# Kernel optimization log

Hardware: AMD Instinct MI355X
Metric: run time of the kernel (lower is better)

The kernel has to match this reference:

```python
import jax, jax.numpy as jnp
import numpy as np

N_HEADS, D_MODEL, D_HEAD = 16, 1024, 64
EPSILON = -100000.0  # module uses -1e5, not -inf
INIT_STD = 0.02


def setup_inputs() -> dict:
    key = jax.random.key(0)
    ks = jax.random.split(key, 5)
    B, S = 4, 2048
    x = jax.random.normal(ks[0], (B, S, D_MODEL), dtype=jnp.float32)
    W_Q = INIT_STD * jax.random.normal(ks[1], (N_HEADS, D_MODEL, D_HEAD), dtype=jnp.float32)
    W_K = INIT_STD * jax.random.normal(ks[2], (N_HEADS, D_MODEL, D_HEAD), dtype=jnp.float32)
    W_V = INIT_STD * jax.random.normal(ks[3], (N_HEADS, D_MODEL, D_HEAD), dtype=jnp.float32)
    W_O = INIT_STD * jax.random.normal(ks[4], (N_HEADS, D_HEAD, D_MODEL), dtype=jnp.float32)
    b_Q = jnp.zeros((N_HEADS, D_HEAD), jnp.float32)
    b_K = jnp.zeros((N_HEADS, D_HEAD), jnp.float32)
    b_V = jnp.zeros((N_HEADS, D_HEAD), jnp.float32)
    b_O = jnp.zeros((D_MODEL,), jnp.float32)
    return {"normalized_resid_pre": x, "W_Q": W_Q, "b_Q": b_Q, "W_K": W_K,
            "b_K": b_K, "W_V": W_V, "b_V": b_V, "W_O": W_O, "b_O": b_O}


def reference(normalized_resid_pre, W_Q, b_Q, W_K, b_K, W_V, b_V, W_O, b_O):
    x = normalized_resid_pre  # [b, s, e]
    q = jnp.einsum('bse,neh->bsnh', x, W_Q) + b_Q
    k = jnp.einsum('bse,neh->bsnh', x, W_K) + b_K
    v = jnp.einsum('bse,neh->bsnh', x, W_V) + b_V
    scores = jnp.einsum('bqnh,bknh->bnqk', q, k) / jnp.sqrt(jnp.float32(D_HEAD))
    sq, sk = scores.shape[-2], scores.shape[-1]
    causal = jnp.triu(jnp.ones((sq, sk), bool), k=1)  # True above diagonal
    scores = jnp.where(causal, jnp.float32(EPSILON), scores)
    probs = jax.nn.softmax(scores, axis=-1)
    z = jnp.einsum('bnqk,bknh->bqnh', probs, v)
    # sum over heads of per-head output projection + bias
    attn_out = jnp.einsum('bqnh,nhe->bqe', z, W_O) + b_O
    return attn_out
```

## Files before the change

### kernel.cpp

```cpp
#include <hip/hip_runtime.h>


typedef __attribute__((ext_vector_type(8))) short short8;
typedef __attribute__((ext_vector_type(4))) float floatx4;

#define SCL 0.1803368801111244f

__device__ __forceinline__ unsigned short f2bf(float f) {
  unsigned int x = __float_as_uint(f);
  x += 0x7fffu + ((x >> 16) & 1u);
  return (unsigned short)(x >> 16);
}

__device__ __forceinline__ void gload_lds16(const unsigned short* g, unsigned short* lds) {
  __builtin_amdgcn_global_load_lds(
      (const __attribute__((address_space(1))) void*)g,
      (__attribute__((address_space(3))) void*)lds, 16, 0, 0);
}

__global__ __launch_bounds__(256) void prep_kernel(
    const float* __restrict__ X,  unsigned short* __restrict__ Xb,
    const float* __restrict__ Wq, const float* __restrict__ Wk,
    const float* __restrict__ Wv, unsigned short* __restrict__ Bt,
    const float* __restrict__ Wo, unsigned short* __restrict__ Wt)
{
  __shared__ unsigned short T[64 * 72];
  const int bid = blockIdx.x, t = threadIdx.x;
  if (bid < 8192) {
    int idx = ((bid << 8) + t) << 2;
    float4 f = *(const float4*)(X + idx);
    unsigned short u[4] = { f2bf(f.x), f2bf(f.y), f2bf(f.z), f2bf(f.w) };
    *(uint2*)(Xb + idx) = *(uint2*)u;
  } else if (bid < 8960) {
    int b2 = bid - 8192;
    int e0 = (b2 & 15) << 6, nn = (b2 >> 4) & 15, proj = b2 >> 8;
    const float* W = (proj == 0) ? Wq : (proj == 1) ? Wk : Wv;
    const float* src = W + ((size_t)nn << 16) + ((size_t)e0 << 6);
#pragma unroll
    for (int rnd = 0; rnd < 4; ++rnd) {
      int off = (rnd << 10) + (t << 2);
      float4 f = *(const float4*)(src + off);
      int r = off >> 6, h = off & 63;
      T[r * 72 + h]     = f2bf(f.x);
      T[r * 72 + h + 1] = f2bf(f.y);
      T[r * 72 + h + 2] = f2bf(f.z);
      T[r * 72 + h + 3] = f2bf(f.w);
    }
    __syncthreads();
    const int h = t >> 2, ck = t & 3;
    size_t orow = ((size_t)((proj << 10) + (nn << 6) + h) << 10) + e0 + (ck << 4);
#pragma unroll
    for (int g = 0; g < 2; ++g) {
      unsigned short v[8];
#pragma unroll
      for (int j = 0; j < 8; ++j) v[j] = T[((ck << 4) + (g << 3) + j) * 72 + h];
      *(int4*)(Bt + orow + (g << 3)) = *(int4*)v;
    }
  } else {
    int b2 = bid - 8960;
    int e0 = (b2 & 15) << 6, k0 = (b2 >> 4) << 6;
#pragma unroll
    for (int rnd = 0; rnd < 4; ++rnd) {
      int r = (rnd << 4) + (t >> 4);
      int c = (t & 15) << 2;
      float4 f = *(const float4*)(Wo + ((size_t)(k0 + r) << 10) + e0 + c);
      T[r * 72 + c]     = f2bf(f.x);
      T[r * 72 + c + 1] = f2bf(f.y);
      T[r * 72 + c + 2] = f2bf(f.z);
      T[r * 72 + c + 3] = f2bf(f.w);
    }
    __syncthreads();
    const int i = t >> 2, ck = t & 3;
    size_t orow = ((size_t)(e0 + i) << 10) + k0 + (ck << 4);
#pragma unroll
    for (int g = 0; g < 2; ++g) {
      unsigned short v[8];
#pragma unroll
      for (int j = 0; j < 8; ++j) v[j] = T[((ck << 4) + (g << 3) + j) * 72 + i];
      *(int4*)(Wt + orow + (g << 3)) = *(int4*)v;
    }
  }
}

template <int MODE>
__global__ __launch_bounds__(256) void gemm128_kernel(
    const unsigned short* __restrict__ A,
    const unsigned short* __restrict__ Bt,
    const float* __restrict__ b0, const float* __restrict__ b1,
    const float* __restrict__ b2,
    unsigned short* __restrict__ Oq, unsigned short* __restrict__ Ok,
    unsigned short* __restrict__ Ov, float* __restrict__ Of)
{
  const int K = 1024;
  __shared__ __align__(16) unsigned short As[8192];
  __shared__ __align__(16) unsigned short Bs[8192];
  const int tid = threadIdx.x;
  const int l   = tid & 63, w = tid >> 6;
  const int l15 = l & 15,  lg = l >> 4;
  const int mo  = (w >> 1) << 6, no = (w & 1) << 6;
  const int m0  = blockIdx.y << 7, n0 = blockIdx.x << 7;
  const int srow = l >> 3;
  const int gblk = ((l & 7) ^ srow) << 3;
  const int rsw  = l15 & 7;

  floatx4 acc[4][4];
#pragma unroll
  for (int i = 0; i < 4; ++i)
#pragma unroll
    for (int j = 0; j < 4; ++j) acc[i][j] = (floatx4){0.f, 0.f, 0.f, 0.f};

  for (int k0 = 0; k0 < K; k0 += 64) {
    __syncthreads();
#pragma unroll
    for (int s = 0; s < 4; ++s) {
      const int br = (s << 5) + (w << 3);
      gload_lds16(A  + (size_t)(m0 + br + srow) * K + k0 + gblk, &As[br << 6]);
      gload_lds16(Bt + (size_t)(n0 + br + srow) * K + k0 + gblk, &Bs[br << 6]);
    }
    __syncthreads();
#pragma unroll
    for (int kh = 0; kh < 2; ++kh) {
      const int bo = (((kh << 2) + lg) ^ rsw) << 3;
      short8 af[4], bf[4];
#pragma unroll
      for (int mc = 0; mc < 4; ++mc)
        af[mc] = *(const short8*)&As[((mo + (mc << 4) + l15) << 6) + bo];
#pragma unroll
      for (int nc = 0; nc < 4; ++nc)
        bf[nc] = *(const short8*)&Bs[((no + (nc << 4) + l15) << 6) + bo];
#pragma unroll
      for (int mc = 0; mc < 4; ++mc)
#pragma unroll
        for (int nc = 0; nc < 4; ++nc)
          acc[mc][nc] = __builtin_amdgcn_mfma_f32_16x16x32_bf16(af[mc], bf[nc], acc[mc][nc], 0, 0, 0);
    }
  }

#pragma unroll
  for (int nc = 0; nc < 4; ++nc) {
    int c = n0 + no + (nc << 4) + l15;
    if (MODE == 1) {
      float bv = b0[c];
#pragma unroll
      for (int mc = 0; mc < 4; ++mc)
#pragma unroll
        for (int r = 0; r < 4; ++r) {
          int m = m0 + mo + (mc << 4) + (lg << 2) + r;
          Of[((size_t)m << 10) + c] = acc[mc][nc][r] + bv;
        }
    } else {
      int proj = c >> 10, cc = c & 1023;
      int hn = cc >> 6, h = cc & 63;
      const float* bp = (proj == 0) ? b0 : (proj == 1) ? b1 : b2;
      float bv = bp[cc];
      float sc = (proj == 0) ? SCL : 1.0f;
      if (proj < 2) {
        unsigned short* O = (proj == 0) ? Oq : Ok;
#pragma unroll
        for (int mc = 0; mc < 4; ++mc)
#pragma unroll
          for (int r = 0; r < 4; ++r) {
            int m = m0 + mo + (mc << 4) + (lg << 2) + r;
            int bb = m >> 11, ss = m & 2047;
            O[((((size_t)(bb << 4) + hn) << 11) + ss) * 64 + h] = f2bf((acc[mc][nc][r] + bv) * sc);
          }
      } else {
#pragma unroll
        for (int mc = 0; mc < 4; ++mc) {
          int m = m0 + mo + (mc << 4) + (lg << 2);
          int bb = m >> 11, ss = m & 2047;
          unsigned short p0 = f2bf(acc[mc][nc][0] + bv);
          unsigned short p1 = f2bf(acc[mc][nc][1] + bv);
          unsigned short p2 = f2bf(acc[mc][nc][2] + bv);
          unsigned short p3 = f2bf(acc[mc][nc][3] + bv);
          uint2 pk;
          pk.x = (unsigned int)p0 | ((unsigned int)p1 << 16);
          pk.y = (unsigned int)p2 | ((unsigned int)p3 << 16);
          *(uint2*)&Ov[((((size_t)(bb << 4) + hn) << 6) + h) * 2048 + ss] = pk;
        }
      }
    }
  }
}

__global__ __launch_bounds__(256, 4) void flash8_kernel(
    const unsigned short* __restrict__ Q,
    const unsigned short* __restrict__ K,
    const unsigned short* __restrict__ Vt,
    unsigned short* __restrict__ Z)
{
  __shared__ __align__(16) unsigned short Ks[8192];
  __shared__ __align__(16) unsigned short Vs[8192];
  __shared__ __align__(16) unsigned short Ps[8192];

  const int tid = threadIdx.x;
  const int l   = tid & 63, w = tid >> 6;
  const int l15 = l & 15,  lg = l >> 4;
  const int x    = blockIdx.x;
  const int qt   = 15 - (x >> 6);
  const int head = x & 63;
  const int n = head & 15, b = head >> 4;
  const size_t hoff = (size_t)head << 17;
  const unsigned short* Qh = Q + hoff;
  const unsigned short* Kh = K + hoff;
  const unsigned short* Vh = Vt + hoff;
  unsigned short* Psw = Ps + (w << 11);

  const int srow8 = l >> 3;
  const int sblk8 = ((l & 7) ^ srow8) << 3;
  const int swz   = l15 & 7;
  const int bo0   = (lg ^ swz) << 3;
  const int bo1   = ((4 + lg) ^ swz) << 3;

  int pwofs[4], profs[2];
#pragma unroll
  for (int mc = 0; mc < 4; ++mc)
    pwofs[mc] = ((((mc << 1) + (lg >> 1)) ^ swz) << 3) + ((lg & 1) << 2);
#pragma unroll
  for (int kc = 0; kc < 2; ++kc)
    profs[kc] = (((kc << 2) + lg) ^ swz) << 3;

  short8 onef;
#pragma unroll
  for (int i = 0; i < 8; ++i) onef[i] = (short)0x3F80;

  const int q0w = (qt << 7) + (w << 5);

  short8 qf[2][2];
#pragma unroll
  for (int qc = 0; qc < 2; ++qc)
#pragma unroll
    for (int dh = 0; dh < 2; ++dh)
      qf[qc][dh] = *(const short8*)(Qh + (size_t)(q0w + (qc << 4) + l15) * 64 + (dh << 5) + (lg << 3));

  floatx4 acc_o[2][4], acc_l[2];
#pragma unroll
  for (int qc = 0; qc < 2; ++qc) {
    acc_l[qc] = (floatx4){0.f, 0.f, 0.f, 0.f};
#pragma unroll
    for (int dc = 0; dc < 4; ++dc) acc_o[qc][dc] = (floatx4){0.f, 0.f, 0.f, 0.f};
  }

#pragma unroll
  for (int j = 0; j < 2; ++j) {
    const int s = (w << 1) + j;
    gload_lds16(Kh + (size_t)((s << 3) + srow8) * 64 + sblk8, &Ks[s << 9]);
    gload_lds16(Vh + (size_t)((s << 3) + srow8) * 2048 + sblk8, &Vs[s << 9]);
  }
  asm volatile("s_waitcnt vmcnt(0)" ::: "memory");
  __builtin_amdgcn_s_barrier();

  int buf = 0;
  const int nkt = (qt << 1) + 2;
  for (int kt = 0; kt < nkt; ++kt) {
    const int k0 = kt << 6;

    if (kt + 1 < nkt) {
      const int nk0 = (kt + 1) << 6;
      const int nb = (buf ^ 1) << 12;
#pragma unroll
      for (int j = 0; j < 2; ++j) {
        const int s = (w << 1) + j;
        gload_lds16(Kh + (size_t)(nk0 + (s << 3) + srow8) * 64 + sblk8, &Ks[nb + (s << 9)]);
        gload_lds16(Vh + (size_t)((s << 3) + srow8) * 2048 + nk0 + sblk8, &Vs[nb + (s << 9)]);
      }
    }

    if (k0 <= q0w + 31) {
      const int cb = buf << 12;

      floatx4 s0[4], s1[4];
#pragma unroll
      for (int mc = 0; mc < 4; ++mc) {
        s0[mc] = (floatx4){0.f, 0.f, 0.f, 0.f};
        s1[mc] = (floatx4){0.f, 0.f, 0.f, 0.f};
      }
      __builtin_amdgcn_s_setprio(1);
#pragma unroll
      for (int dh = 0; dh < 2; ++dh) {
        const int bo = dh ? bo1 : bo0;
#pragma unroll
        for (int mc = 0; mc < 4; ++mc) {
          short8 ak = *(const short8*)&Ks[cb + (((mc << 4) + l15) << 6) + bo];
          s0[mc] = __builtin_amdgcn_mfma_f32_16x16x32_bf16(ak, qf[0][dh], s0[mc], 0, 0, 0);
          s1[mc] = __builtin_amdgcn_mfma_f32_16x16x32_bf16(ak, qf[1][dh], s1[mc], 0, 0, 0);
        }
      }
      __builtin_amdgcn_s_setprio(0);

      const bool needmask = (k0 + 63 > q0w);
#pragma unroll
      for (int qc = 0; qc < 2; ++qc) {
        const int qg = q0w + (qc << 4) + l15;
        const int rbase = ((qc << 4) + l15) << 6;
#pragma unroll
        for (int mc = 0; mc < 4; ++mc) {
          float p[4];
#pragma unroll
          for (int r = 0; r < 4; ++r) {
            float e = exp2f(qc ? s1[mc][r] : s0[mc][r]);
            if (needmask) {
              int key = k0 + (mc << 4) + (lg << 2) + r;
              e = (key > qg) ? 0.f : e;
            }
            p[r] = e;
          }
          uint2 pk;
          pk.x = (__float_as_uint(p[1]) & 0xFFFF0000u) | (__float_as_uint(p[0]) >> 16);
          pk.y = (__float_as_uint(p[3]) & 0xFFFF0000u) | (__float_as_uint(p[2]) >> 16);
          *(uint2*)&Psw[rbase + pwofs[mc]] = pk;
        }
      }

      short8 pa[2][2];
#pragma unroll
      for (int qc = 0; qc < 2; ++qc) {
        const int rbase = ((qc << 4) + l15) << 6;
#pragma unroll
        for (int kc = 0; kc < 2; ++kc)
          pa[qc][kc] = *(const short8*)&Psw[rbase + profs[kc]];
      }
      __builtin_amdgcn_s_setprio(1);
#pragma unroll
      for (int kc = 0; kc < 2; ++kc) {
        const int bo = kc ? bo1 : bo0;
#pragma unroll
        for (int dc = 0; dc < 4; ++dc) {
          short8 vb = *(const short8*)&Vs[cb + (((dc << 4) + l15) << 6) + bo];
          acc_o[0][dc] = __builtin_amdgcn_mfma_f32_16x16x32_bf16(pa[0][kc], vb, acc_o[0][dc], 0, 0, 0);
          acc_o[1][dc] = __builtin_amdgcn_mfma_f32_16x16x32_bf16(pa[1][kc], vb, acc_o[1][dc], 0, 0, 0);
        }
        acc_l[0] = __builtin_amdgcn_mfma_f32_16x16x32_bf16(pa[0][kc], onef, acc_l[0], 0, 0, 0);
        acc_l[1] = __builtin_amdgcn_mfma_f32_16x16x32_bf16(pa[1][kc], onef, acc_l[1], 0, 0, 0);
      }
      __builtin_amdgcn_s_setprio(0);
    }

    asm volatile("s_waitcnt vmcnt(0)" ::: "memory");
    __builtin_amdgcn_s_barrier();
    buf ^= 1;
  }

#pragma unroll
  for (int qc = 0; qc < 2; ++qc) {
    floatx4 inv;
#pragma unroll
    for (int r = 0; r < 4; ++r) inv[r] = 1.f / acc_l[qc][r];
#pragma unroll
    for (int dc = 0; dc < 4; ++dc)
#pragma unroll
      for (int r = 0; r < 4; ++r) {
        int qg = q0w + (qc << 4) + (lg << 2) + r;
        Z[(((size_t)b << 11) + qg) * 1024 + (n << 6) + (dc << 4) + l15] =
            f2bf(acc_o[qc][dc][r] * inv[r]);
      }
  }
}

extern "C" void kernel_launch(void* const* d_in, const int* in_sizes, int n_in,
                              void* d_out, int out_size, void* d_ws, size_t ws_size,
                              hipStream_t stream) {
  const float* x   = (const float*)d_in[0];
  const float* W_Q = (const float*)d_in[1];
  const float* b_Q = (const float*)d_in[2];
  const float* W_K = (const float*)d_in[3];
  const float* b_K = (const float*)d_in[4];
  const float* W_V = (const float*)d_in[5];
  const float* b_V = (const float*)d_in[6];
  const float* W_O = (const float*)d_in[7];
  const float* b_O = (const float*)d_in[8];
  float* out = (float*)d_out;

  unsigned short* ws    = (unsigned short*)d_ws;
  unsigned short* BtQKV = ws;
  unsigned short* Wo_t  = BtQKV + (3u << 20);
  unsigned short* Xb    = Wo_t + (1u << 20);
  unsigned short* Qb    = Xb + (8u << 20);
  unsigned short* Kb    = Qb + (8u << 20);
  unsigned short* Vtb   = Kb + (8u << 20);
  unsigned short* Zb    = Vtb + (8u << 20);

  prep_kernel<<<9216, 256, 0, stream>>>(x, Xb, W_Q, W_K, W_V, BtQKV, W_O, Wo_t);

  gemm128_kernel<0><<<dim3(24, 64), 256, 0, stream>>>(
      Xb, BtQKV, b_Q, b_K, b_V, Qb, Kb, Vtb, nullptr);

  flash8_kernel<<<1024, 256, 0, stream>>>(Qb, Kb, Vtb, Zb);

  gemm128_kernel<1><<<dim3(8, 64), 256, 0, stream>>>(
      Zb, Wo_t, b_O, nullptr, nullptr, nullptr, nullptr, nullptr, out);
}
```

Measured before the change: 274.9 us.

## Single-buffer V tile loaded during QK^T phase with mid-iteration barrier

The flash attention kernel now keeps only one V tile in LDS. That tile is loaded at the start of each iteration so its fetch overlaps the QK^T and softmax work, and a barrier is placed before the PV phase, while K stays double-buffered. It also uses v_cvt_pk_bf16_f32 for packing P, which rounds rather than truncates as the old bit-masking did, and precomputes the P pointers. The QK^T accumulation starts from a zero register instead of zero-initialised accumulators. The aim is to cut LDS usage and address arithmetic, at the cost of a second barrier per iteration and exposing V load latency if the score phase is short.

Result: faster. 263.4 us (-4.2%).

```diff
diff --git a/kernel.cpp b/kernel.cpp
--- a/kernel.cpp
+++ b/kernel.cpp
@@ -183,14 +183,14 @@
   }
 }
 
-__global__ __launch_bounds__(256, 4) void flash8_kernel(
+__global__ __launch_bounds__(256, 4) void flash9_kernel(
     const unsigned short* __restrict__ Q,
     const unsigned short* __restrict__ K,
     const unsigned short* __restrict__ Vt,
     unsigned short* __restrict__ Z)
 {
   __shared__ __align__(16) unsigned short Ks[8192];
-  __shared__ __align__(16) unsigned short Vs[8192];
+  __shared__ __align__(16) unsigned short Vs[4096];
   __shared__ __align__(16) unsigned short Ps[8192];
 
   const int tid = threadIdx.x;
@@ -212,17 +212,30 @@
   const int bo0   = (lg ^ swz) << 3;
   const int bo1   = ((4 + lg) ^ swz) << 3;
 
-  int pwofs[4], profs[2];
-#pragma unroll
-  for (int mc = 0; mc < 4; ++mc)
-    pwofs[mc] = ((((mc << 1) + (lg >> 1)) ^ swz) << 3) + ((lg & 1) << 2);
-#pragma unroll
-  for (int kc = 0; kc < 2; ++kc)
-    profs[kc] = (((kc << 2) + lg) ^ swz) << 3;
+  const unsigned short* gK = Kh + (size_t)(((w << 4) + srow8) << 6) + sblk8;
+  const unsigned short* gV = Vh + (size_t)(((w << 4) + srow8) << 11) + sblk8;
+  unsigned short* ldsK0 = &Ks[w << 10];
+  unsigned short* ldsV0 = &Vs[w << 10];
+
+  uint2* pw[2][4];
+  const short8* pr[2][2];
+#pragma unroll
+  for (int qc = 0; qc < 2; ++qc) {
+    const int rbase = ((qc << 4) + l15) << 6;
+#pragma unroll
+    for (int mc = 0; mc < 4; ++mc)
+      pw[qc][mc] = (uint2*)&Psw[rbase + (((((mc << 1) + (lg >> 1)) ^ swz) << 3) + ((lg & 1) << 2))];
+#pragma unroll
+    for (int kc = 0; kc < 2; ++kc)
+      pr[qc][kc] = (const short8*)&Psw[rbase + ((((kc << 2) + lg) ^ swz) << 3)];
+  }
 
   short8 onef;
 #pragma unroll
   for (int i = 0; i < 8; ++i) onef[i] = (short)0x3F80;
+
+  floatx4 z4 = (floatx4){0.f, 0.f, 0.f, 0.f};
+  asm volatile("" : "+v"(z4));
 
   const int q0w = (qt << 7) + (w << 5);
 
@@ -241,12 +254,8 @@
     for (int dc = 0; dc < 4; ++dc) acc_o[qc][dc] = (floatx4){0.f, 0.f, 0.f, 0.f};
   }
 
-#pragma unroll
-  for (int j = 0; j < 2; ++j) {
-    const int s = (w << 1) + j;
-    gload_lds16(Kh + (size_t)((s << 3) + srow8) * 64 + sblk8, &Ks[s << 9]);
-    gload_lds16(Vh + (size_t)((s << 3) + srow8) * 2048 + sblk8, &Vs[s << 9]);
-  }
+  gload_lds16(gK,       ldsK0);
+  gload_lds16(gK + 512, ldsK0 + 512);
   asm volatile("s_waitcnt vmcnt(0)" ::: "memory");
   __builtin_amdgcn_s_barrier();
 
@@ -255,36 +264,35 @@
   for (int kt = 0; kt < nkt; ++kt) {
     const int k0 = kt << 6;
 
+    {
+      const unsigned short* pV = gV + k0;
+      gload_lds16(pV,          ldsV0);
+      gload_lds16(pV + 16384,  ldsV0 + 512);
+    }
     if (kt + 1 < nkt) {
-      const int nk0 = (kt + 1) << 6;
-      const int nb = (buf ^ 1) << 12;
-#pragma unroll
-      for (int j = 0; j < 2; ++j) {
-        const int s = (w << 1) + j;
-        gload_lds16(Kh + (size_t)(nk0 + (s << 3) + srow8) * 64 + sblk8, &Ks[nb + (s << 9)]);
-        gload_lds16(Vh + (size_t)((s << 3) + srow8) * 2048 + nk0 + sblk8, &Vs[nb + (s << 9)]);
-      }
-    }
-
-    if (k0 <= q0w + 31) {
+      const unsigned short* pK = gK + ((size_t)(kt + 1) << 12);
+      unsigned short* d = ldsK0 + ((buf ^ 1) << 12);
+      gload_lds16(pK,       d);
+      gload_lds16(pK + 512, d + 512);
+    }
+
+    const bool active = (k0 <= q0w + 31);
+    if (active) {
       const int cb = buf << 12;
 
       floatx4 s0[4], s1[4];
+      __builtin_amdgcn_s_setprio(1);
 #pragma unroll
       for (int mc = 0; mc < 4; ++mc) {
-        s0[mc] = (floatx4){0.f, 0.f, 0.f, 0.f};
-        s1[mc] = (floatx4){0.f, 0.f, 0.f, 0.f};
-      }
-      __builtin_amdgcn_s_setprio(1);
-#pragma unroll
-      for (int dh = 0; dh < 2; ++dh) {
-        const int bo = dh ? bo1 : bo0;
-#pragma unroll
-        for (int mc = 0; mc < 4; ++mc) {
-          short8 ak = *(const short8*)&Ks[cb + (((mc << 4) + l15) << 6) + bo];
-          s0[mc] = __builtin_amdgcn_mfma_f32_16x16x32_bf16(ak, qf[0][dh], s0[mc], 0, 0, 0);
-          s1[mc] = __builtin_amdgcn_mfma_f32_16x16x32_bf16(ak, qf[1][dh], s1[mc], 0, 0, 0);
-        }
+        short8 ak = *(const short8*)&Ks[cb + (((mc << 4) + l15) << 6) + bo0];
+        s0[mc] = __builtin_amdgcn_mfma_f32_16x16x32_bf16(ak, qf[0][0], z4, 0, 0, 0);
+        s1[mc] = __builtin_amdgcn_mfma_f32_16x16x32_bf16(ak, qf[1][0], z4, 0, 0, 0);
+      }
+#pragma unroll
+      for (int mc = 0; mc < 4; ++mc) {
+        short8 ak = *(const short8*)&Ks[cb + (((mc << 4) + l15) << 6) + bo1];
+        s0[mc] = __builtin_amdgcn_mfma_f32_16x16x32_bf16(ak, qf[0][1], s0[mc], 0, 0, 0);
+        s1[mc] = __builtin_amdgcn_mfma_f32_16x16x32_bf16(ak, qf[1][1], s1[mc], 0, 0, 0);
       }
       __builtin_amdgcn_s_setprio(0);
 
@@ -292,7 +300,6 @@
 #pragma unroll
       for (int qc = 0; qc < 2; ++qc) {
         const int qg = q0w + (qc << 4) + l15;
-        const int rbase = ((qc << 4) + l15) << 6;
 #pragma unroll
         for (int mc = 0; mc < 4; ++mc) {
           float p[4];
@@ -306,27 +313,30 @@
             p[r] = e;
           }
           uint2 pk;
-          pk.x = (__float_as_uint(p[1]) & 0xFFFF0000u) | (__float_as_uint(p[0]) >> 16);
-          pk.y = (__float_as_uint(p[3]) & 0xFFFF0000u) | (__float_as_uint(p[2]) >> 16);
-          *(uint2*)&Psw[rbase + pwofs[mc]] = pk;
+          asm("v_cvt_pk_bf16_f32 %0, %1, %2" : "=v"(pk.x) : "v"(p[0]), "v"(p[1]));
+          asm("v_cvt_pk_bf16_f32 %0, %1, %2" : "=v"(pk.y) : "v"(p[2]), "v"(p[3]));
+          *pw[qc][mc] = pk;
         }
       }
-
+    }
+
+    asm volatile("s_waitcnt vmcnt(0)" ::: "memory");
+    __builtin_amdgcn_s_barrier();
+
+    if (active) {
       short8 pa[2][2];
 #pragma unroll
-      for (int qc = 0; qc < 2; ++qc) {
-        const int rbase = ((qc << 4) + l15) << 6;
+      for (int qc = 0; qc < 2; ++qc)
 #pragma unroll
         for (int kc = 0; kc < 2; ++kc)
-          pa[qc][kc] = *(const short8*)&Psw[rbase + profs[kc]];
-      }
+          pa[qc][kc] = *pr[qc][kc];
       __builtin_amdgcn_s_setprio(1);
 #pragma unroll
       for (int kc = 0; kc < 2; ++kc) {
         const int bo = kc ? bo1 : bo0;
 #pragma unroll
         for (int dc = 0; dc < 4; ++dc) {
-          short8 vb = *(const short8*)&Vs[cb + (((dc << 4) + l15) << 6) + bo];
+          short8 vb = *(const short8*)&Vs[(((dc << 4) + l15) << 6) + bo];
           acc_o[0][dc] = __builtin_amdgcn_mfma_f32_16x16x32_bf16(pa[0][kc], vb, acc_o[0][dc], 0, 0, 0);
           acc_o[1][dc] = __builtin_amdgcn_mfma_f32_16x16x32_bf16(pa[1][kc], vb, acc_o[1][dc], 0, 0, 0);
         }
@@ -336,7 +346,6 @@
       __builtin_amdgcn_s_setprio(0);
     }
 
-    asm volatile("s_waitcnt vmcnt(0)" ::: "memory");
     __builtin_amdgcn_s_barrier();
     buf ^= 1;
   }
@@ -385,7 +394,7 @@
   gemm128_kernel<0><<<dim3(24, 64), 256, 0, stream>>>(
       Xb, BtQKV, b_Q, b_K, b_V, Qb, Kb, Vtb, nullptr);
 
-  flash8_kernel<<<1024, 256, 0, stream>>>(Qb, Kb, Vtb, Zb);
+  flash9_kernel<<<1024, 256, 0, stream>>>(Qb, Kb, Vtb, Zb);
 
   gemm128_kernel<1><<<dim3(8, 64), 256, 0, stream>>>(
       Zb, Wo_t, b_O, nullptr, nullptr, nullptr, nullptr, nullptr, out);
```
